# Kernel optimization log

Measured on AMD Instinct MI355X. Metric: run time of the kernel, lower is better.

The kernel has to match this reference:

```python
import jax, jax.numpy as jnp
import numpy as np

N, E, MSG, HID, T, C = 100000, 1600000, 16, 16, 8, 32

def setup_inputs() -> dict:
    key = jax.random.key(0)
    ks = jax.random.split(key, 12)
    return {
        'features': jax.random.normal(ks[0], (N, HID), dtype=jnp.float32),
        'src': jax.random.randint(ks[1], (E,), 0, N, dtype=jnp.int32),
        'dst': jax.random.randint(ks[2], (E,), 0, N, dtype=jnp.int32),
        'etype': jax.random.randint(ks[3], (E,), 0, T, dtype=jnp.int32),
        'edge_table': jax.random.normal(ks[4], (T, MSG * HID), dtype=jnp.float32) * 0.1,
        'W_ih': jax.random.normal(ks[5], (3 * HID, MSG), dtype=jnp.float32) * 0.1,
        'W_hh': jax.random.normal(ks[6], (3 * HID, HID), dtype=jnp.float32) * 0.1,
        'b_ih': jax.random.normal(ks[7], (3 * HID,), dtype=jnp.float32) * 0.1,
        'b_hh': jax.random.normal(ks[8], (3 * HID,), dtype=jnp.float32) * 0.1,
        'W_out': jax.random.normal(ks[9], (C, HID), dtype=jnp.float32) * 0.1,
        'b_out': jax.random.normal(ks[10], (C,), dtype=jnp.float32) * 0.1,
    }

def reference(features, src, dst, etype, edge_table, W_ih, W_hh, b_ih, b_hh, W_out, b_out):
    n_nodes, hid = features.shape
    msg_dim = edge_table.shape[1] // hid
    # per-edge message matrix lookup: [E, msg, hid]
    A = edge_table[etype].reshape(-1, msg_dim, hid)
    # msg = A @ h_src : [E, msg]
    msg = jnp.einsum('emh,eh->em', A, features[src])
    # scatter-sum into destination nodes: [N, msg]
    m = jax.ops.segment_sum(msg, dst, num_segments=n_nodes)
    # single GRU step (PyTorch gate ordering: r, z, n)
    gi = m @ W_ih.T + b_ih          # [N, 3*hid]
    gh = features @ W_hh.T + b_hh   # [N, 3*hid]
    i_r, i_z, i_n = jnp.split(gi, 3, axis=1)
    h_r, h_z, h_n = jnp.split(gh, 3, axis=1)
    r = jax.nn.sigmoid(i_r + h_r)
    z = jax.nn.sigmoid(i_z + h_z)
    n = jnp.tanh(i_n + r * h_n)
    h = (1.0 - z) * n + z * features
    # output projection
    return h @ W_out.T + b_out
```

## Files before the change

kernel.cpp:

```cpp
#include <hip/hip_runtime.h>
#include <hip/hip_fp16.h>

#define N_NODES 100000
#define N_EDGES 1600000
#define MSG 16
#define HID 16
#define NT 8
#define NC 32
#define PREP_N 800000

typedef _Float16 v2h __attribute__((ext_vector_type(2)));

union H2U {
    v2h h;
    unsigned int u;
};

__global__ __launch_bounds__(256) void ggnn_prep(
    const float* __restrict__ feat,
    unsigned int* __restrict__ feat16,
    unsigned int* __restrict__ m2) {
    int i = blockIdx.x * 256 + threadIdx.x;
    if (i >= PREP_N) return;
    float2 f = reinterpret_cast<const float2*>(feat)[i];
    H2U p;
    p.h[0] = (_Float16)f.x;
    p.h[1] = (_Float16)f.y;
    feat16[i] = p.u;
    m2[i] = 0u;
}

__global__ __launch_bounds__(256) void ggnn_edge(
    const int* __restrict__ src,
    const int* __restrict__ dst,
    const int* __restrict__ etype,
    const unsigned int* __restrict__ feat16,
    const float* __restrict__ edge_table,
    unsigned int* __restrict__ m2) {
    __shared__ float As[NT * MSG * HID];
    int tid = threadIdx.x;
    #pragma unroll
    for (int i = tid; i < NT * MSG * HID; i += 256) {
        int t = i >> 8;
        int k = (i >> 4) & 15;
        int j = i & 15;
        As[i] = edge_table[t * 256 + j * 16 + k];
    }
    __syncthreads();

    int grp = tid >> 4;
    int j = tid & 15;
    int g = grp & 3;
    int stride = gridDim.x * 16;

    for (int e = blockIdx.x * 16 + grp; e < N_EDGES; e += stride) {
        int s = src[e];
        int t = etype[e];
        H2U hp;
        hp.u = feat16[s * 8 + (j >> 1)];
        float hj = (float)hp.h[j & 1];

        const float* At = As + t * 256;
        float acc = 0.f;
        #pragma unroll
        for (int k0 = 0; k0 < 16; ++k0) {
            int k = (k0 + g) & 15;
            float hk = __shfl(hj, k, 16);
            acc += At[k * 16 + j] * hk;
        }

        int d = dst[e];
        float a = __shfl(acc, 2 * (j & 7), 16);
        float b = __shfl(acc, 2 * (j & 7) + 1, 16);
        if (j < 8) {
            H2U p;
            p.h[0] = (_Float16)a;
            p.h[1] = (_Float16)b;
            __builtin_amdgcn_global_atomic_fadd_v2f16(
                reinterpret_cast<v2h*>(m2 + (size_t)d * 8 + j), p.h);
        }
    }
}

__device__ __forceinline__ float fast_sigmoid(float x) {
    return 1.f / (1.f + __expf(-x));
}
__device__ __forceinline__ float fast_tanh(float x) {
    return 2.f / (1.f + __expf(-2.f * x)) - 1.f;
}

__global__ __launch_bounds__(256) void ggnn_node(
    const float* __restrict__ feat,
    const unsigned int* __restrict__ m2,
    const float* __restrict__ W_ih,
    const float* __restrict__ W_hh,
    const float* __restrict__ b_ih,
    const float* __restrict__ b_hh,
    const float* __restrict__ W_out,
    const float* __restrict__ b_out,
    float* __restrict__ out) {
    int n = blockIdx.x * 256 + threadIdx.x;
    if (n >= N_NODES) return;

    float mv[MSG], h[HID];
    {
        const uint4* mu = reinterpret_cast<const uint4*>(m2 + (size_t)n * 8);
        uint4 a = mu[0], b = mu[1];
        unsigned int w[8] = {a.x, a.y, a.z, a.w, b.x, b.y, b.z, b.w};
        #pragma unroll
        for (int i = 0; i < 8; ++i) {
            H2U hh;
            hh.u = w[i];
            mv[2 * i]     = (float)hh.h[0];
            mv[2 * i + 1] = (float)hh.h[1];
        }
        const float4* f4 = reinterpret_cast<const float4*>(feat + (size_t)n * HID);
        #pragma unroll
        for (int q = 0; q < 4; ++q) {
            float4 v = f4[q];
            h[q * 4 + 0] = v.x; h[q * 4 + 1] = v.y;
            h[q * 4 + 2] = v.z; h[q * 4 + 3] = v.w;
        }
    }

    float srz[2 * HID];
    for (int g = 0; g < 2 * HID; ++g) {
        float ai = 0.f, ah = 0.f;
        const float* wi = W_ih + g * MSG;
        const float* wh = W_hh + g * HID;
        #pragma unroll
        for (int k = 0; k < HID; ++k) {
            ai += wi[k] * mv[k];
            ah += wh[k] * h[k];
        }
        srz[g] = ai + ah + b_ih[g] + b_hh[g];
    }
    float i_n[HID], h_n[HID];
    #pragma unroll
    for (int j = 0; j < HID; ++j) {
        int g = 2 * HID + j;
        float ai = b_ih[g], ah = b_hh[g];
        const float* wi = W_ih + g * MSG;
        const float* wh = W_hh + g * HID;
        #pragma unroll
        for (int k = 0; k < HID; ++k) {
            ai += wi[k] * mv[k];
            ah += wh[k] * h[k];
        }
        i_n[j] = ai;
        h_n[j] = ah;
    }

    float hn[HID];
    #pragma unroll
    for (int j = 0; j < HID; ++j) {
        float r = fast_sigmoid(srz[j]);
        float z = fast_sigmoid(srz[HID + j]);
        float nn = fast_tanh(i_n[j] + r * h_n[j]);
        hn[j] = (1.f - z) * nn + z * h[j];
    }

    float4* op = reinterpret_cast<float4*>(out + (size_t)n * NC);
    #pragma unroll
    for (int c4 = 0; c4 < NC / 4; ++c4) {
        float4 o;
        float* oo = &o.x;
        #pragma unroll
        for (int cc = 0; cc < 4; ++cc) {
            int c = c4 * 4 + cc;
            float acc = b_out[c];
            const float* wo = W_out + c * HID;
            #pragma unroll
            for (int k = 0; k < HID; ++k) acc += wo[k] * hn[k];
            oo[cc] = acc;
        }
        op[c4] = o;
    }
}

extern "C" void kernel_launch(void* const* d_in, const int* in_sizes, int n_in,
                              void* d_out, int out_size, void* d_ws, size_t ws_size,
                              hipStream_t stream) {
    const float* feat       = (const float*)d_in[0];
    const int*   src        = (const int*)d_in[1];
    const int*   dst        = (const int*)d_in[2];
    const int*   etype      = (const int*)d_in[3];
    const float* edge_table = (const float*)d_in[4];
    const float* W_ih       = (const float*)d_in[5];
    const float* W_hh       = (const float*)d_in[6];
    const float* b_ih       = (const float*)d_in[7];
    const float* b_hh       = (const float*)d_in[8];
    const float* W_out      = (const float*)d_in[9];
    const float* b_out      = (const float*)d_in[10];
    float* out = (float*)d_out;

    unsigned int* m2     = (unsigned int*)d_ws;
    unsigned int* feat16 = m2 + (size_t)N_NODES * 8;

    int pblocks = (PREP_N + 255) / 256;
    ggnn_prep<<<pblocks, 256, 0, stream>>>(feat, feat16, m2);

    ggnn_edge<<<2048, 256, 0, stream>>>(src, dst, etype, feat16, edge_table, m2);

    int nblocks = (N_NODES + 255) / 256;
    ggnn_node<<<nblocks, 256, 0, stream>>>(feat, m2, W_ih, W_hh, b_ih, b_hh,
                                           W_out, b_out, out);
}
```

Before: 240.9 us.

## Restructure edge kernel to 8 threads per edge with fp16 dot2 products

The edge kernel now assigns 8 threads per edge, each computing two message outputs with packed fp16 dot2 instructions over vector-loaded source features and an fp16-converted edge table. This replaces the shared-memory table, the 16-lane shuffle reduction and the grid-stride loop. The table is converted to fp16 in the prep kernel and read from global/L1 instead of LDS. It trades shuffle and LDS traffic for more threads and uint4 loads, and accumulating in fp16 dot2 adds some precision risk.

After: 201.2 us. -16.5%, faster.

```diff
diff --git a/kernel.cpp b/kernel.cpp
--- a/kernel.cpp
+++ b/kernel.cpp
@@ -8,6 +8,7 @@
 #define NT 8
 #define NC 32
 #define PREP_N 800000
+#define A2_WORDS 1024
 
 typedef _Float16 v2h __attribute__((ext_vector_type(2)));
 
@@ -16,18 +17,45 @@
     unsigned int u;
 };
 
+__device__ __forceinline__ float dot2acc(unsigned int a, unsigned int b, float acc) {
+    H2U x, y;
+    x.u = a; y.u = b;
+#if __has_builtin(__builtin_amdgcn_fdot2)
+    return __builtin_amdgcn_fdot2(x.h, y.h, acc, false);
+#else
+    return acc + (float)x.h[0] * (float)y.h[0] + (float)x.h[1] * (float)y.h[1];
+#endif
+}
+
+__device__ __forceinline__ float fast_sigmoid(float x) {
+    return 1.f / (1.f + __expf(-x));
+}
+__device__ __forceinline__ float fast_tanh(float x) {
+    return 2.f / (1.f + __expf(-2.f * x)) - 1.f;
+}
+
 __global__ __launch_bounds__(256) void ggnn_prep(
     const float* __restrict__ feat,
+    const float* __restrict__ edge_table,
     unsigned int* __restrict__ feat16,
-    unsigned int* __restrict__ m2) {
+    unsigned int* __restrict__ m2,
+    unsigned int* __restrict__ A2) {
     int i = blockIdx.x * 256 + threadIdx.x;
-    if (i >= PREP_N) return;
-    float2 f = reinterpret_cast<const float2*>(feat)[i];
-    H2U p;
-    p.h[0] = (_Float16)f.x;
-    p.h[1] = (_Float16)f.y;
-    feat16[i] = p.u;
-    m2[i] = 0u;
+    if (i < PREP_N) {
+        float2 f = reinterpret_cast<const float2*>(feat)[i];
+        H2U p;
+        p.h[0] = (_Float16)f.x;
+        p.h[1] = (_Float16)f.y;
+        feat16[i] = p.u;
+        m2[i] = 0u;
+    }
+    if (i < A2_WORDS) {
+        float2 f = reinterpret_cast<const float2*>(edge_table)[i];
+        H2U p;
+        p.h[0] = (_Float16)f.x;
+        p.h[1] = (_Float16)f.y;
+        A2[i] = p.u;
+    }
 }
 
 __global__ __launch_bounds__(256) void ggnn_edge(
@@ -35,58 +63,38 @@
     const int* __restrict__ dst,
     const int* __restrict__ etype,
     const unsigned int* __restrict__ feat16,
-    const float* __restrict__ edge_table,
+    const unsigned int* __restrict__ A2,
     unsigned int* __restrict__ m2) {
-    __shared__ float As[NT * MSG * HID];
-    int tid = threadIdx.x;
-    #pragma unroll
-    for (int i = tid; i < NT * MSG * HID; i += 256) {
-        int t = i >> 8;
-        int k = (i >> 4) & 15;
-        int j = i & 15;
-        As[i] = edge_table[t * 256 + j * 16 + k];
-    }
-    __syncthreads();
-
-    int grp = tid >> 4;
-    int j = tid & 15;
-    int g = grp & 3;
-    int stride = gridDim.x * 16;
-
-    for (int e = blockIdx.x * 16 + grp; e < N_EDGES; e += stride) {
-        int s = src[e];
-        int t = etype[e];
-        H2U hp;
-        hp.u = feat16[s * 8 + (j >> 1)];
-        float hj = (float)hp.h[j & 1];
-
-        const float* At = As + t * 256;
-        float acc = 0.f;
-        #pragma unroll
-        for (int k0 = 0; k0 < 16; ++k0) {
-            int k = (k0 + g) & 15;
-            float hk = __shfl(hj, k, 16);
-            acc += At[k * 16 + j] * hk;
-        }
-
-        int d = dst[e];
-        float a = __shfl(acc, 2 * (j & 7), 16);
-        float b = __shfl(acc, 2 * (j & 7) + 1, 16);
-        if (j < 8) {
-            H2U p;
-            p.h[0] = (_Float16)a;
-            p.h[1] = (_Float16)b;
-            __builtin_amdgcn_global_atomic_fadd_v2f16(
-                reinterpret_cast<v2h*>(m2 + (size_t)d * 8 + j), p.h);
-        }
-    }
-}
-
-__device__ __forceinline__ float fast_sigmoid(float x) {
-    return 1.f / (1.f + __expf(-x));
-}
-__device__ __forceinline__ float fast_tanh(float x) {
-    return 2.f / (1.f + __expf(-2.f * x)) - 1.f;
+    int tid = blockIdx.x * 256 + threadIdx.x;
+    int e = tid >> 3;
+    if (e >= N_EDGES) return;
+    int c = tid & 7;
+
+    int s = src[e];
+    int t = etype[e];
+    const uint4* hp = reinterpret_cast<const uint4*>(feat16 + (size_t)s * 8);
+    uint4 h0 = hp[0], h1 = hp[1];
+    const uint4* ap = reinterpret_cast<const uint4*>(A2 + t * 128 + c * 16);
+    uint4 a0 = ap[0], a1 = ap[1], a2 = ap[2], a3 = ap[3];
+
+    float r0 = 0.f, r1 = 0.f;
+    r0 = dot2acc(h0.x, a0.x, r0); r0 = dot2acc(h0.y, a0.y, r0);
+    r0 = dot2acc(h0.z, a0.z, r0); r0 = dot2acc(h0.w, a0.w, r0);
+    r0 = dot2acc(h1.x, a1.x, r0); r0 = dot2acc(h1.y, a1.y, r0);
+    r0 = dot2acc(h1.z, a1.z, r0); r0 = dot2acc(h1.w, a1.w, r0);
+    r1 = dot2acc(h0.x, a2.x, r1); r1 = dot2acc(h0.y, a2.y, r1);
+    r1 = dot2acc(h0.z, a2.z, r1); r1 = dot2acc(h0.w, a2.w, r1);
+    r1 = dot2acc(h1.x, a3.x, r1); r1 = dot2acc(h1.y, a3.y, r1);
+    r1 = dot2acc(h1.z, a3.z, r1); r1 = dot2acc(h1.w, a3.w, r1);
+
+    int d = dst[e];
+    H2U p;
+    p.h[0] = (_Float16)r0;
+    p.h[1] = (_Float16)r1;
+#if __has_builtin(__builtin_amdgcn_global_atomic_fadd_v2f16)
+    __builtin_amdgcn_global_atomic_fadd_v2f16(
+        reinterpret_cast<v2h*>(m2 + (size_t)d * 8 + c), p.h);
+#endif
 }
 
 __global__ __launch_bounds__(256) void ggnn_node(
@@ -195,12 +203,15 @@
     float* out = (float*)d_out;
 
     unsigned int* m2     = (unsigned int*)d_ws;
-    unsigned int* feat16 = m2 + (size_t)N_NODES * 8;
+    unsigned int* feat16 = m2 + PREP_N;
+    unsigned int* A2     = feat16 + PREP_N;
 
     int pblocks = (PREP_N + 255) / 256;
-    ggnn_prep<<<pblocks, 256, 0, stream>>>(feat, feat16, m2);
-
-    ggnn_edge<<<2048, 256, 0, stream>>>(src, dst, etype, feat16, edge_table, m2);
+    ggnn_prep<<<pblocks, 256, 0, stream>>>(feat, edge_table, feat16, m2, A2);
+
+    long long ethreads = (long long)N_EDGES * 8;
+    int eblocks = (int)((ethreads + 255) / 256);
+    ggnn_edge<<<eblocks, 256, 0, stream>>>(src, dst, etype, feat16, A2, m2);
 
     int nblocks = (N_NODES + 255) / 256;
     ggnn_node<<<nblocks, 256, 0, stream>>>(feat, m2, W_ih, W_hh, b_ih, b_hh,
```
